# Performance work log

Measured on AMD Instinct MI355X. Metric: run time of the kernel, lower is better.

## Reference

```python
import jax, jax.numpy as jnp
import numpy as np

EMBED_DIM = 1024
NUM_HEADS = 16
HEAD_DIM = EMBED_DIM // NUM_HEADS


def setup_inputs() -> dict:
    key = jax.random.key(0)
    k_x, k_qw, k_qb, k_ow, k_ob = jax.random.split(key, 5)
    C = EMBED_DIM
    # torch nn.Linear init scale ~ U(-1/sqrt(fan_in), 1/sqrt(fan_in)); use small normals
    s = 1.0 / np.sqrt(C)
    return {
        "x": jax.random.normal(k_x, (4, 2048, C), dtype=jnp.float32),
        "qkv_w": jax.random.uniform(k_qw, (3 * C, C), jnp.float32, -s, s),
        "qkv_b": jax.random.uniform(k_qb, (3 * C,), jnp.float32, -s, s),
        "fc_w": jax.random.uniform(k_ow, (C, C), jnp.float32, -s, s),
        "fc_b": jax.random.uniform(k_ob, (C,), jnp.float32, -s, s),
    }


def reference(x, qkv_w, qkv_b, fc_w, fc_b):
    B, N, C = x.shape
    H, D = NUM_HEADS, HEAD_DIM
    scale = D ** -0.5
    qkv = x @ qkv_w.T + qkv_b                      # [B,N,3C]
    qkv = qkv.reshape(B, N, 3, H, D)
    q, k, v = [jnp.transpose(qkv[:, :, i], (0, 2, 1, 3)) for i in range(3)]  # [B,H,N,D]
    attn = jnp.einsum("bhqd,bhkd->bhqk", q, k) * scale
    attn = jax.nn.softmax(attn, axis=-1)
    out = jnp.einsum("bhqk,bhkd->bhqd", attn, v)   # [B,H,N,D]
    out = jnp.transpose(out, (0, 2, 1, 3)).reshape(B, N, C)
    return out @ fc_w.T + fc_b
```

## Files before the change

kernel.cpp:

```cpp
#include <hip/hip_runtime.h>

#define NUM_HEADS 16
#define HEAD_DIM  64
#define EMB       1024
#define SEQ       2048
#define BATCH     4
#define MROWS     (BATCH * SEQ)
#define QKV_ELEMS (MROWS * EMB)

typedef __attribute__((ext_vector_type(4))) float  floatx4;
typedef __attribute__((ext_vector_type(8))) __bf16 bf16x8;

__device__ __forceinline__ unsigned short f2bf(float f) {
    unsigned int u = __float_as_uint(f);
    u += 0x7fffu + ((u >> 16) & 1u);
    return (unsigned short)(u >> 16);
}

__device__ __forceinline__ ushort4 pk4(float4 v) {
    return make_ushort4(f2bf(v.x), f2bf(v.y), f2bf(v.z), f2bf(v.w));
}

__device__ __forceinline__ uint2 packbf4(float a0, float a1, float a2, float a3) {
    unsigned r0 = __float_as_uint(a0) + 0x8000u;
    unsigned r1 = __float_as_uint(a1) + 0x8000u;
    unsigned r2 = __float_as_uint(a2) + 0x8000u;
    unsigned r3 = __float_as_uint(a3) + 0x8000u;
    uint2 r;
    r.x = __builtin_amdgcn_perm(r1, r0, 0x07060302u);
    r.y = __builtin_amdgcn_perm(r3, r2, 0x07060302u);
    return r;
}

#define MFMA16(a, b, c) __builtin_amdgcn_mfma_f32_16x16x32_bf16((a), (b), (c), 0, 0, 0)

__device__ __forceinline__ void async16(const unsigned short* g, unsigned short* l) {
    __builtin_amdgcn_global_load_lds((const __attribute__((address_space(1))) void*)g,
                                     (__attribute__((address_space(3))) void*)l,
                                     16, 0, 0);
}

#define QSCALE 0.18033688011112042f

#define XV4  2097152
#define QWV4 786432
#define FWV4 262144

__global__ __launch_bounds__(256)
void convert_kernel(const float* __restrict__ x, const float* __restrict__ qw,
                    const float* __restrict__ fw,
                    unsigned short* __restrict__ xb, unsigned short* __restrict__ qwb,
                    unsigned short* __restrict__ fwb)
{
    const size_t i = (size_t)blockIdx.x * 256 + threadIdx.x;
    const float* src; unsigned short* dst; size_t off;
    if (i < XV4)              { src = x;  dst = xb;  off = i; }
    else if (i < XV4 + QWV4)  { src = qw; dst = qwb; off = i - XV4; }
    else                      { src = fw; dst = fwb; off = i - (XV4 + QWV4); }
    float4 v = ((const float4*)src)[off];
    ((ushort4*)dst)[off] = pk4(v);
}

__global__ __launch_bounds__(256, 3)
void qkv_kernel(const unsigned short* __restrict__ X, const unsigned short* __restrict__ W,
                const float* __restrict__ BIAS,
                unsigned short* __restrict__ qb, unsigned short* __restrict__ kb,
                unsigned short* __restrict__ vtb)
{
    __shared__ unsigned short As[128 * 32];
    __shared__ unsigned short Bs[128 * 32];

    const int t    = threadIdx.x;
    const int n0   = blockIdx.x * 128;
    const int m0   = blockIdx.y * 128;
    const int wave = t >> 6, lane = t & 63;
    const int wm   = wave & 1, wn = wave >> 1;
    const int l15  = lane & 15, quad = lane >> 4;

    const int srow = wave * 32 + (lane >> 2);
    const int scol = (lane & 3) * 8;
    const unsigned short* gA = X + (size_t)(m0 + srow) * EMB + scol;
    const unsigned short* gB = W + (size_t)(n0 + srow) * EMB + scol;
    unsigned short* lA = &As[srow * 32 + scol];
    unsigned short* lB = &Bs[srow * 32 + scol];

    const floatx4 zero4 = {0.f, 0.f, 0.f, 0.f};
    floatx4 acc[4][4];
    #pragma unroll
    for (int i = 0; i < 4; ++i)
        #pragma unroll
        for (int j = 0; j < 4; ++j) acc[i][j] = zero4;

    for (int k0 = 0; k0 < EMB; k0 += 32) {
        __syncthreads();
        async16(gA + k0,                     lA);
        async16(gA + k0 + (size_t)16 * EMB,  lA + 16 * 32);
        async16(gB + k0,                     lB);
        async16(gB + k0 + (size_t)16 * EMB,  lB + 16 * 32);
        __syncthreads();

        bf16x8 af[4], bfv[4];
        #pragma unroll
        for (int i = 0; i < 4; ++i) {
            af[i]  = *(const bf16x8*)&As[(wm * 64 + i * 16 + l15) * 32 + quad * 8];
            bfv[i] = *(const bf16x8*)&Bs[(wn * 64 + i * 16 + l15) * 32 + quad * 8];
        }
        #pragma unroll
        for (int mi = 0; mi < 4; ++mi)
            #pragma unroll
            for (int ni = 0; ni < 4; ++ni)
                acc[mi][ni] = MFMA16(af[mi], bfv[ni], acc[mi][ni]);
    }

    const int bb = m0 >> 11;
    #pragma unroll
    for (int ni = 0; ni < 4; ++ni) {
        const int gc     = n0 + wn * 64 + ni * 16 + l15;
        const float bias = BIAS[gc];
        const int which  = gc >> 10;
        const int rem    = gc & 1023;
        const int hh     = rem >> 6;
        const int dd     = rem & 63;
        #pragma unroll
        for (int mi = 0; mi < 4; ++mi) {
            const int nseq0 = (m0 & 2047) + wm * 64 + mi * 16 + quad * 4;
            floatx4 v = acc[mi][ni];
            if (which == 2) {
                ushort4 pk;
                pk.x = f2bf(v[0] + bias); pk.y = f2bf(v[1] + bias);
                pk.z = f2bf(v[2] + bias); pk.w = f2bf(v[3] + bias);
                *(ushort4*)&vtb[((size_t)(bb * NUM_HEADS + hh) * HEAD_DIM + dd) * SEQ + nseq0] = pk;
            } else {
                unsigned short* dst = which ? kb : qb;
                const float sc = which ? 1.0f : QSCALE;
                #pragma unroll
                for (int r = 0; r < 4; ++r)
                    dst[((size_t)(bb * NUM_HEADS + hh) * SEQ + (nseq0 + r)) * HEAD_DIM + dd] =
                        f2bf((v[r] + bias) * sc);
            }
        }
    }
}

__global__ __launch_bounds__(256, 2)
void attn_kernel(const unsigned short* __restrict__ qb, const unsigned short* __restrict__ kb,
                 const unsigned short* __restrict__ vtb, unsigned short* __restrict__ attnb)
{
    __shared__ unsigned short smem[32768];

    const int t    = threadIdx.x;
    const int bh   = blockIdx.x;
    const int q0   = blockIdx.y * 128;
    const int b    = bh >> 4, h = bh & 15;
    const int wave = t >> 6, lane = t & 63;
    const int l15  = lane & 15, quad = lane >> 4;
    const int srow = lane >> 2;
    const int scol = (lane & 3) * 8;

    const unsigned short* qp = qb  + (size_t)bh * SEQ * HEAD_DIM;
    const unsigned short* kp = kb  + (size_t)bh * SEQ * HEAD_DIM;
    const unsigned short* vp = vtb + (size_t)bh * HEAD_DIM * SEQ;

    {
        const int r0 = wave * 32 + srow;
        async16(qp + (size_t)(q0 + r0) * 64 + scol,           &smem[16384 + r0 * 32 + scol]);
        async16(qp + (size_t)(q0 + r0 + 16) * 64 + scol,      &smem[16384 + (r0 + 16) * 32 + scol]);
        async16(qp + (size_t)(q0 + r0) * 64 + 32 + scol,      &smem[20480 + r0 * 32 + scol]);
        async16(qp + (size_t)(q0 + r0 + 16) * 64 + 32 + scol, &smem[20480 + (r0 + 16) * 32 + scol]);
    }
    __syncthreads();
    bf16x8 qf[2][2];
    #pragma unroll
    for (int qi = 0; qi < 2; ++qi)
        #pragma unroll
        for (int kk = 0; kk < 2; ++kk)
            qf[qi][kk] = *(const bf16x8*)&smem[16384 + kk * 4096 +
                         (wave * 32 + qi * 16 + l15) * 32 + quad * 8];

    bf16x8 ones;
    #pragma unroll
    for (int i = 0; i < 8; ++i) ones[i] = (__bf16)1.0f;

    const floatx4 zero4 = {0.f, 0.f, 0.f, 0.f};
    floatx4 o[2][4], o_sum[2];
    #pragma unroll
    for (int mi = 0; mi < 2; ++mi) {
        o_sum[mi] = zero4;
        #pragma unroll
        for (int ni = 0; ni < 4; ++ni) o[mi][ni] = zero4;
    }
    unsigned short* Pw = &smem[16384 + wave * 4096];

    for (int kv0 = 0; kv0 < SEQ; kv0 += 128) {
        __syncthreads();
        {
            const int kr = wave * 32 + srow;
            async16(kp + (size_t)(kv0 + kr) * 64 + scol,           &smem[kr * 32 + scol]);
            async16(kp + (size_t)(kv0 + kr + 16) * 64 + scol,      &smem[(kr + 16) * 32 + scol]);
            async16(kp + (size_t)(kv0 + kr) * 64 + 32 + scol,      &smem[4096 + kr * 32 + scol]);
            async16(kp + (size_t)(kv0 + kr + 16) * 64 + 32 + scol, &smem[4096 + (kr + 16) * 32 + scol]);
            const int vd = wave * 16 + srow;
            #pragma unroll
            for (int kk = 0; kk < 4; ++kk)
                async16(vp + (size_t)vd * SEQ + kv0 + kk * 32 + scol,
                        &smem[8192 + kk * 2048 + vd * 32 + scol]);
        }
        __syncthreads();

        floatx4 st[8][2];
        #pragma unroll
        for (int sub = 0; sub < 8; ++sub) { st[sub][0] = zero4; st[sub][1] = zero4; }
        #pragma unroll
        for (int sub = 0; sub < 8; ++sub)
            #pragma unroll
            for (int kk = 0; kk < 2; ++kk) {
                bf16x8 kf = *(const bf16x8*)&smem[kk * 4096 +
                            (sub * 16 + l15) * 32 + quad * 8];
                st[sub][0] = MFMA16(kf, qf[0][kk], st[sub][0]);
                st[sub][1] = MFMA16(kf, qf[1][kk], st[sub][1]);
            }

        uint2 pku[2][8];
        #pragma unroll
        for (int qi = 0; qi < 2; ++qi)
            #pragma unroll
            for (int sub = 0; sub < 8; ++sub)
                pku[qi][sub] = packbf4(exp2f(st[sub][qi][0]), exp2f(st[sub][qi][1]),
                                       exp2f(st[sub][qi][2]), exp2f(st[sub][qi][3]));

        #pragma unroll
        for (int qi = 0; qi < 2; ++qi)
            #pragma unroll
            for (int sub = 0; sub < 8; ++sub) {
                const int kkk = sub >> 1;
                const int pos = (((sub & 1) << 2) | quad) ^ (l15 & 6);
                *(uint2*)&Pw[kkk * 1024 + (qi * 16 + l15) * 32 + pos * 4] = pku[qi][sub];
            }

        #pragma unroll
        for (int kk = 0; kk < 4; ++kk) {
            bf16x8 pf[2];
            const int p0 = (2 * quad) ^ (l15 & 6);
            #pragma unroll
            for (int mi = 0; mi < 2; ++mi)
                pf[mi] = *(const bf16x8*)&Pw[kk * 1024 + (mi * 16 + l15) * 32 + p0 * 4];
            #pragma unroll
            for (int ni = 0; ni < 4; ++ni) {
                bf16x8 vf = *(const bf16x8*)&smem[8192 + kk * 2048 +
                            (ni * 16 + l15) * 32 + quad * 8];
                o[0][ni] = MFMA16(pf[0], vf, o[0][ni]);
                o[1][ni] = MFMA16(pf[1], vf, o[1][ni]);
            }
            o_sum[0] = MFMA16(pf[0], ones, o_sum[0]);
            o_sum[1] = MFMA16(pf[1], ones, o_sum[1]);
        }
    }

    #pragma unroll
    for (int mi = 0; mi < 2; ++mi)
        #pragma unroll
        for (int r = 0; r < 4; ++r) {
            const float inv = 1.0f / o_sum[mi][r];
            const int qrow  = q0 + wave * 32 + mi * 16 + quad * 4 + r;
            #pragma unroll
            for (int ni = 0; ni < 4; ++ni)
                attnb[(size_t)(b * SEQ + qrow) * EMB + h * HEAD_DIM + ni * 16 + l15] =
                    f2bf(o[mi][ni][r] * inv);
        }
}

__global__ __launch_bounds__(256, 3)
void proj_kernel(const unsigned short* __restrict__ A, const unsigned short* __restrict__ W,
                 const float* __restrict__ BIAS, float* __restrict__ out)
{
    __shared__ unsigned short As[128 * 32];
    __shared__ unsigned short Bs[128 * 32];

    const int t    = threadIdx.x;
    const int n0   = blockIdx.x * 128;
    const int m0   = blockIdx.y * 128;
    const int wave = t >> 6, lane = t & 63;
    const int wm   = wave & 1, wn = wave >> 1;
    const int l15  = lane & 15, quad = lane >> 4;

    const int srow = wave * 32 + (lane >> 2);
    const int scol = (lane & 3) * 8;
    const unsigned short* gA = A + (size_t)(m0 + srow) * EMB + scol;
    const unsigned short* gB = W + (size_t)(n0 + srow) * EMB + scol;
    unsigned short* lA = &As[srow * 32 + scol];
    unsigned short* lB = &Bs[srow * 32 + scol];

    const floatx4 zero4 = {0.f, 0.f, 0.f, 0.f};
    floatx4 acc[4][4];
    #pragma unroll
    for (int i = 0; i < 4; ++i)
        #pragma unroll
        for (int j = 0; j < 4; ++j) acc[i][j] = zero4;

    for (int k0 = 0; k0 < EMB; k0 += 32) {
        __syncthreads();
        async16(gA + k0,                     lA);
        async16(gA + k0 + (size_t)16 * EMB,  lA + 16 * 32);
        async16(gB + k0,                     lB);
        async16(gB + k0 + (size_t)16 * EMB,  lB + 16 * 32);
        __syncthreads();

        bf16x8 af[4], bfv[4];
        #pragma unroll
        for (int i = 0; i < 4; ++i) {
            af[i]  = *(const bf16x8*)&As[(wm * 64 + i * 16 + l15) * 32 + quad * 8];
            bfv[i] = *(const bf16x8*)&Bs[(wn * 64 + i * 16 + l15) * 32 + quad * 8];
        }
        #pragma unroll
        for (int mi = 0; mi < 4; ++mi)
            #pragma unroll
            for (int ni = 0; ni < 4; ++ni)
                acc[mi][ni] = MFMA16(af[mi], bfv[ni], acc[mi][ni]);
    }

    #pragma unroll
    for (int ni = 0; ni < 4; ++ni) {
        const int gc     = n0 + wn * 64 + ni * 16 + l15;
        const float bias = BIAS[gc];
        #pragma unroll
        for (int mi = 0; mi < 4; ++mi) {
            const int gm = m0 + wm * 64 + mi * 16 + quad * 4;
            #pragma unroll
            for (int r = 0; r < 4; ++r)
                out[(size_t)(gm + r) * EMB + gc] = acc[mi][ni][r] + bias;
        }
    }
}

extern "C" void kernel_launch(void* const* d_in, const int* in_sizes, int n_in,
                              void* d_out, int out_size, void* d_ws, size_t ws_size,
                              hipStream_t stream) {
    (void)in_sizes; (void)n_in; (void)out_size; (void)ws_size;
    const float* x     = (const float*)d_in[0];
    const float* qkv_w = (const float*)d_in[1];
    const float* qkv_b = (const float*)d_in[2];
    const float* fc_w  = (const float*)d_in[3];
    const float* fc_b  = (const float*)d_in[4];
    float* out = (float*)d_out;

    unsigned short* xb    = (unsigned short*)d_ws;
    unsigned short* attnb = xb;
    unsigned short* qbuf  = xb    + QKV_ELEMS;
    unsigned short* kbuf  = qbuf  + QKV_ELEMS;
    unsigned short* vtbuf = kbuf  + QKV_ELEMS;
    unsigned short* qwb   = vtbuf + QKV_ELEMS;
    unsigned short* fwb   = qwb   + 3 * EMB * EMB;

    convert_kernel<<<dim3((XV4 + QWV4 + FWV4) / 256), 256, 0, stream>>>(
        x, qkv_w, fc_w, xb, qwb, fwb);
    qkv_kernel<<<dim3(24, 64), 256, 0, stream>>>(xb, qwb, qkv_b, qbuf, kbuf, vtbuf);
    attn_kernel<<<dim3(64, 16), 256, 0, stream>>>(qbuf, kbuf, vtbuf, attnb);
    proj_kernel<<<dim3(8, 64), 256, 0, stream>>>(attnb, fwb, fc_b, out);
}
```

Before: 304.6 us.

## Switch attention to 32x32 MFMA and keep P in registers via lane shuffles

The attention kernel now uses 32x32x16 bf16 MFMA tiles in place of 16x16x32 for both QK^T and PV. The S accumulator layout is reused directly as the A operand for PV by exchanging halves across lanes with a shuffle, so P no longer round-trips through LDS. This drops the LDS writes and reads for P and shrinks shared memory. In exchange it adds cross-lane shuffles, and the larger 16-float accumulators raise register pressure.

```diff
diff --git a/kernel.cpp b/kernel.cpp
--- a/kernel.cpp
+++ b/kernel.cpp
@@ -8,8 +8,9 @@
 #define MROWS     (BATCH * SEQ)
 #define QKV_ELEMS (MROWS * EMB)
 
-typedef __attribute__((ext_vector_type(4))) float  floatx4;
-typedef __attribute__((ext_vector_type(8))) __bf16 bf16x8;
+typedef __attribute__((ext_vector_type(4)))  float  floatx4;
+typedef __attribute__((ext_vector_type(16))) float  floatx16;
+typedef __attribute__((ext_vector_type(8)))  __bf16 bf16x8;
 
 __device__ __forceinline__ unsigned short f2bf(float f) {
     unsigned int u = __float_as_uint(f);
@@ -32,7 +33,14 @@
     return r;
 }
 
+__device__ __forceinline__ bf16x8 mk8(uint2 lo, uint2 hi) {
+    union { uint4 u; bf16x8 b; } cvt;
+    cvt.u = make_uint4(lo.x, lo.y, hi.x, hi.y);
+    return cvt.b;
+}
+
 #define MFMA16(a, b, c) __builtin_amdgcn_mfma_f32_16x16x32_bf16((a), (b), (c), 0, 0, 0)
+#define MFMA32(a, b, c) __builtin_amdgcn_mfma_f32_32x32x16_bf16((a), (b), (c), 0, 0, 0)
 
 __device__ __forceinline__ void async16(const unsigned short* g, unsigned short* l) {
     __builtin_amdgcn_global_load_lds((const __attribute__((address_space(1))) void*)g,
@@ -146,14 +154,14 @@
 void attn_kernel(const unsigned short* __restrict__ qb, const unsigned short* __restrict__ kb,
                  const unsigned short* __restrict__ vtb, unsigned short* __restrict__ attnb)
 {
-    __shared__ unsigned short smem[32768];
+    __shared__ unsigned short smem[24576];
 
     const int t    = threadIdx.x;
     const int bh   = blockIdx.x;
     const int q0   = blockIdx.y * 128;
-    const int b    = bh >> 4, h = bh & 15;
+    const int b    = bh >> 4, hh = bh & 15;
     const int wave = t >> 6, lane = t & 63;
-    const int l15  = lane & 15, quad = lane >> 4;
+    const int l31  = lane & 31, hl = lane >> 5;
     const int srow = lane >> 2;
     const int scol = (lane & 3) * 8;
 
@@ -169,27 +177,19 @@
         async16(qp + (size_t)(q0 + r0 + 16) * 64 + 32 + scol, &smem[20480 + (r0 + 16) * 32 + scol]);
     }
     __syncthreads();
-    bf16x8 qf[2][2];
-    #pragma unroll
-    for (int qi = 0; qi < 2; ++qi)
-        #pragma unroll
-        for (int kk = 0; kk < 2; ++kk)
-            qf[qi][kk] = *(const bf16x8*)&smem[16384 + kk * 4096 +
-                         (wave * 32 + qi * 16 + l15) * 32 + quad * 8];
+    bf16x8 qf[4];
+    #pragma unroll
+    for (int ks = 0; ks < 4; ++ks)
+        qf[ks] = *(const bf16x8*)&smem[16384 + (ks >> 1) * 4096 +
+                 (wave * 32 + l31) * 32 + (ks & 1) * 16 + hl * 8];
 
     bf16x8 ones;
     #pragma unroll
     for (int i = 0; i < 8; ++i) ones[i] = (__bf16)1.0f;
 
-    const floatx4 zero4 = {0.f, 0.f, 0.f, 0.f};
-    floatx4 o[2][4], o_sum[2];
-    #pragma unroll
-    for (int mi = 0; mi < 2; ++mi) {
-        o_sum[mi] = zero4;
-        #pragma unroll
-        for (int ni = 0; ni < 4; ++ni) o[mi][ni] = zero4;
-    }
-    unsigned short* Pw = &smem[16384 + wave * 4096];
+    floatx16 o[2], o_sum;
+    #pragma unroll
+    for (int i = 0; i < 16; ++i) { o[0][i] = 0.f; o[1][i] = 0.f; o_sum[i] = 0.f; }
 
     for (int kv0 = 0; kv0 < SEQ; kv0 += 128) {
         __syncthreads();
@@ -207,65 +207,54 @@
         }
         __syncthreads();
 
-        floatx4 st[8][2];
-        #pragma unroll
-        for (int sub = 0; sub < 8; ++sub) { st[sub][0] = zero4; st[sub][1] = zero4; }
-        #pragma unroll
-        for (int sub = 0; sub < 8; ++sub)
-            #pragma unroll
-            for (int kk = 0; kk < 2; ++kk) {
-                bf16x8 kf = *(const bf16x8*)&smem[kk * 4096 +
-                            (sub * 16 + l15) * 32 + quad * 8];
-                st[sub][0] = MFMA16(kf, qf[0][kk], st[sub][0]);
-                st[sub][1] = MFMA16(kf, qf[1][kk], st[sub][1]);
+        #pragma unroll
+        for (int tt = 0; tt < 4; ++tt) {
+            floatx16 st;
+            #pragma unroll
+            for (int i = 0; i < 16; ++i) st[i] = 0.f;
+            #pragma unroll
+            for (int ks = 0; ks < 4; ++ks) {
+                bf16x8 kf = *(const bf16x8*)&smem[(ks >> 1) * 4096 +
+                            (tt * 32 + l31) * 32 + (ks & 1) * 16 + hl * 8];
+                st = MFMA32(kf, qf[ks], st);
             }
-
-        uint2 pku[2][8];
-        #pragma unroll
-        for (int qi = 0; qi < 2; ++qi)
-            #pragma unroll
-            for (int sub = 0; sub < 8; ++sub)
-                pku[qi][sub] = packbf4(exp2f(st[sub][qi][0]), exp2f(st[sub][qi][1]),
-                                       exp2f(st[sub][qi][2]), exp2f(st[sub][qi][3]));
-
-        #pragma unroll
-        for (int qi = 0; qi < 2; ++qi)
-            #pragma unroll
-            for (int sub = 0; sub < 8; ++sub) {
-                const int kkk = sub >> 1;
-                const int pos = (((sub & 1) << 2) | quad) ^ (l15 & 6);
-                *(uint2*)&Pw[kkk * 1024 + (qi * 16 + l15) * 32 + pos * 4] = pku[qi][sub];
+            uint2 pk0 = packbf4(exp2f(st[0]),  exp2f(st[1]),  exp2f(st[2]),  exp2f(st[3]));
+            uint2 pk1 = packbf4(exp2f(st[4]),  exp2f(st[5]),  exp2f(st[6]),  exp2f(st[7]));
+            uint2 pk2 = packbf4(exp2f(st[8]),  exp2f(st[9]),  exp2f(st[10]), exp2f(st[11]));
+            uint2 pk3 = packbf4(exp2f(st[12]), exp2f(st[13]), exp2f(st[14]), exp2f(st[15]));
+
+            uint2 xa = hl ? pk0 : pk1;
+            xa.x = __shfl_xor(xa.x, 32); xa.y = __shfl_xor(xa.y, 32);
+            bf16x8 pfA = hl ? mk8(xa, pk1) : mk8(pk0, xa);
+            uint2 xb2 = hl ? pk2 : pk3;
+            xb2.x = __shfl_xor(xb2.x, 32); xb2.y = __shfl_xor(xb2.y, 32);
+            bf16x8 pfB = hl ? mk8(xb2, pk3) : mk8(pk2, xb2);
+
+            #pragma unroll
+            for (int s = 0; s < 2; ++s) {
+                const bf16x8 pf   = s ? pfB : pfA;
+                const int kvblk   = tt * 2 + s;
+                const int qoff    = 8192 + (kvblk >> 1) * 2048 + (kvblk & 1) * 16 + hl * 8;
+                #pragma unroll
+                for (int dt = 0; dt < 2; ++dt) {
+                    bf16x8 vf = *(const bf16x8*)&smem[qoff + (dt * 32 + l31) * 32];
+                    o[dt] = MFMA32(pf, vf, o[dt]);
+                }
+                o_sum = MFMA32(pf, ones, o_sum);
             }
-
-        #pragma unroll
-        for (int kk = 0; kk < 4; ++kk) {
-            bf16x8 pf[2];
-            const int p0 = (2 * quad) ^ (l15 & 6);
-            #pragma unroll
-            for (int mi = 0; mi < 2; ++mi)
-                pf[mi] = *(const bf16x8*)&Pw[kk * 1024 + (mi * 16 + l15) * 32 + p0 * 4];
-            #pragma unroll
-            for (int ni = 0; ni < 4; ++ni) {
-                bf16x8 vf = *(const bf16x8*)&smem[8192 + kk * 2048 +
-                            (ni * 16 + l15) * 32 + quad * 8];
-                o[0][ni] = MFMA16(pf[0], vf, o[0][ni]);
-                o[1][ni] = MFMA16(pf[1], vf, o[1][ni]);
-            }
-            o_sum[0] = MFMA16(pf[0], ones, o_sum[0]);
-            o_sum[1] = MFMA16(pf[1], ones, o_sum[1]);
-        }
-    }
-
-    #pragma unroll
-    for (int mi = 0; mi < 2; ++mi)
-        #pragma unroll
-        for (int r = 0; r < 4; ++r) {
-            const float inv = 1.0f / o_sum[mi][r];
-            const int qrow  = q0 + wave * 32 + mi * 16 + quad * 4 + r;
-            #pragma unroll
-            for (int ni = 0; ni < 4; ++ni)
-                attnb[(size_t)(b * SEQ + qrow) * EMB + h * HEAD_DIM + ni * 16 + l15] =
-                    f2bf(o[mi][ni][r] * inv);
+        }
+    }
+
+    #pragma unroll
+    for (int g = 0; g < 4; ++g)
+        #pragma unroll
+        for (int e = 0; e < 4; ++e) {
+            const float inv  = 1.0f / o_sum[g * 4 + e];
+            const int  qrow  = q0 + wave * 32 + e + g * 8 + hl * 4;
+            #pragma unroll
+            for (int dt = 0; dt < 2; ++dt)
+                attnb[(size_t)(b * SEQ + qrow) * EMB + hh * HEAD_DIM + dt * 32 + l31] =
+                    f2bf(o[dt][g * 4 + e] * inv);
         }
 }
 
```

Measured after the change: 311.1 us. 1.02x slower.
